# Kernel tuning notes

Measured on AMD Instinct MI355X. Metric: run time of the kernel, lower is better.

## Reference

```python
import jax, jax.numpy as jnp
import numpy as np
from math import sqrt

B, L, D, H, DK, IN = 128, 256, 128, 4, 64, 40
N = B * L
E = 524288
NLAYERS = 4
DISW = 1.5
EPS = 1e-5


def _ln(x, g, b):
    mu = x.mean(-1, keepdims=True)
    v = ((x - mu) ** 2).mean(-1, keepdims=True)
    return (x - mu) / jnp.sqrt(v + EPS) * g + b


def setup_inputs() -> dict:
    key = jax.random.key(0)
    ks = jax.random.split(key, 32)
    x = jax.random.normal(ks[0], (N, IN), jnp.float32)
    # equal-sized graphs: graph g owns nodes [g*L, (g+1)*L)
    e_per = E // B
    off = (jnp.arange(E) // e_per) * L
    src = off + jax.random.randint(ks[1], (E,), 0, L)
    dst = off + jax.random.randint(ks[2], (E,), 0, L)
    edge_index = jnp.stack([src, dst]).astype(jnp.int32)
    edge_attr = jax.random.uniform(ks[3], (E,), jnp.float32)
    # adjacency-type matrix with entries in {0, 1, 1.2} as in the source's adj semantics
    a = jax.random.randint(ks[4], (B, L, L), 0, 3)
    adj = jnp.where(a == 2, 1.2, a.astype(jnp.float32))
    dis = jax.random.randint(ks[5], (B, L, L), 0, 7).astype(jnp.float32)
    mask = jnp.ones((B, L), dtype=bool)  # all graphs have length L -> no padding
    s = 0.05
    p = {}
    p['gnn0_rel_w'] = jax.random.normal(ks[6], (IN, D)) * s
    p['gnn0_rel_b'] = jnp.zeros((D,), jnp.float32)
    p['gnn0_root_w'] = jax.random.normal(ks[7], (IN, D)) * s
    p['gnn_rel_w'] = jax.random.normal(ks[8], (NLAYERS - 1, D, D)) * s
    p['gnn_rel_b'] = jnp.zeros((NLAYERS - 1, D), jnp.float32)
    p['gnn_root_w'] = jax.random.normal(ks[9], (NLAYERS - 1, D, D)) * s
    p['nm_g'] = jnp.ones((NLAYERS, D), jnp.float32)
    p['nm_b'] = jnp.zeros((NLAYERS, D), jnp.float32)
    p['wq'] = jax.random.normal(ks[10], (NLAYERS, D, H * DK)) * s
    p['wk'] = jax.random.normal(ks[11], (NLAYERS, D, H * DK)) * s
    p['wv'] = jax.random.normal(ks[12], (NLAYERS, D, H * DK)) * s
    p['fc'] = jax.random.normal(ks[13], (NLAYERS, H * DK, D)) * s
    p['mha_ln_g'] = jnp.ones((NLAYERS, D), jnp.float32)
    p['mha_ln_b'] = jnp.zeros((NLAYERS, D), jnp.float32)
    p['enc_ln_g'] = jnp.ones((NLAYERS, D), jnp.float32)
    p['enc_ln_b'] = jnp.zeros((NLAYERS, D), jnp.float32)
    p['proj_w'] = jax.random.normal(ks[14], (D, D)) * s
    p['proj_b'] = jnp.zeros((D,), jnp.float32)
    return dict(x=x, edge_index=edge_index, edge_attr=edge_attr, adj=adj, dis=dis, mask=mask, **p)


def _graph_conv(x, src, dst, ew, rel_w, rel_b, root_w):
    # torch_geometric GraphConv: lin_rel(sum_j e_ji * x_j) + lin_root(x_i)
    msg = ew[:, None] * x[src]
    agg = jax.ops.segment_sum(msg, dst, num_segments=N)
    return agg @ rel_w + rel_b + x @ root_w


def _encoder(xb, pad, matrix, wq, wk, wv, fc, mg, mb, eg, eb):
    q = (xb @ wq).reshape(B, L, H, DK).transpose(0, 2, 1, 3)  # [B,H,L,dk]
    k = (xb @ wk).reshape(B, L, H, DK).transpose(0, 2, 1, 3)
    v = (xb @ wv).reshape(B, L, H, DK).transpose(0, 2, 1, 3)
    scores = jnp.einsum('bhqd,bhkd->bhqk', q, k) / sqrt(DK) * matrix[:, None]
    scores = jnp.where(pad[:, None, None, :], -1e9, scores)
    attn = jax.nn.softmax(scores, axis=-1)
    ctx = jnp.einsum('bhqk,bhkd->bhqd', attn, v).transpose(0, 2, 1, 3).reshape(B, L, H * DK)
    out = _ln(ctx @ fc, mg, mb)  # MHA output LayerNorm (dropout is eval -> identity)
    return _ln(out + xb, eg, eb)  # EncoderLayer residual + LayerNorm


def reference(x, edge_index, edge_attr, adj, dis, mask,
              gnn0_rel_w, gnn0_rel_b, gnn0_root_w,
              gnn_rel_w, gnn_rel_b, gnn_root_w,
              nm_g, nm_b, wq, wk, wv, fc,
              mha_ln_g, mha_ln_b, enc_ln_g, enc_ln_b,
              proj_w, proj_b):
    src, dst = edge_index[0], edge_index[1]
    # matrix construction (done once; same matrix_pad reused every layer)
    adj_ = jnp.where(adj == 1.2, 1.1, adj)
    dis_ = jnp.where(dis == 0.0, 0.0, 1.0 / jnp.power(DISW, dis - 1.0))
    matrix = jnp.where(adj == 0.0, dis_, adj_)  # [B,L,L]
    pad = ~mask  # key padding mask (True = masked); all-False here
    h = x
    for i in range(NLAYERS):
        rw = gnn0_rel_w if i == 0 else gnn_rel_w[i - 1]
        rb = gnn0_rel_b if i == 0 else gnn_rel_b[i - 1]
        ow = gnn0_root_w if i == 0 else gnn_root_w[i - 1]
        h = _graph_conv(h, src, dst, edge_attr, rw, rb, ow)
        h = jax.nn.relu(_ln(h, nm_g[i], nm_b[i]))
        xb = h.reshape(B, L, D)  # to_dense_batch with equal lengths
        xb = _encoder(xb, pad, matrix, wq[i], wk[i], wv[i], fc[i],
                      mha_ln_g[i], mha_ln_b[i], enc_ln_g[i], enc_ln_b[i])
        h = xb.reshape(N, D)  # masked_select back to node list
    return h @ proj_w + proj_b
```

## Files before the change

### kernel.cpp

```cpp
#include <hip/hip_runtime.h>
#include <stdint.h>

typedef unsigned short u16;
typedef unsigned int u32;
typedef __attribute__((ext_vector_type(4))) float f32x4;
typedef __attribute__((ext_vector_type(8))) short bf16x8;

#define NB 128
#define LL 256
#define DD 128
#define EDGES 524288
#define EPG 4096
#define NN (NB*LL)

__device__ __forceinline__ float bf2f(u16 u) {
    union { u32 i; float f; } v; v.i = ((u32)u) << 16; return v.f;
}
__device__ __forceinline__ u16 f2bf(float f) {
    union { float f; u32 i; } v; v.f = f;
    u32 i = v.i;
    u32 r = (i + 0x7fffu + ((i >> 16) & 1u)) >> 16;
    return (u16)r;
}
__device__ __forceinline__ float matfn(float a, float dv) {
    if (a != 0.f) return (a == 1.2f) ? 1.1f : a;
    return (dv == 0.f) ? 0.f : exp2f((1.f - dv) * 0.5849625007211562f);
}
__device__ __forceinline__ float red16(float v) {
#pragma unroll
    for (int off = 1; off < 16; off <<= 1) v += __shfl_xor(v, off, 64);
    return v;
}
__device__ __forceinline__ u32 cvtpk(float lo, float hi) {
    u32 r;
    asm("v_cvt_pk_bf16_f32 %0, %1, %2" : "=v"(r) : "v"(lo), "v"(hi));
    return r;
}
__device__ __forceinline__ u32 bperm(int srcLane, u32 v) {
    return (u32)__builtin_amdgcn_ds_bpermute(srcLane << 2, (int)v);
}


__global__ __launch_bounds__(256) void zero_f32(float* __restrict__ p, int n) {
    int i = blockIdx.x * 256 + threadIdx.x;
    if (i < n) p[i] = 0.f;
}

__global__ __launch_bounds__(256) void scatter_w_k(const int* __restrict__ srcI,
                                                   const int* __restrict__ dstI,
                                                   const float* __restrict__ ew,
                                                   float* __restrict__ Wf) {
    int e = blockIdx.x * 256 + threadIdx.x;
    if (e >= EDGES) return;
    int b = e >> 12;
    atomicAdd(&Wf[(size_t)b * 65536 + (size_t)(dstI[e] & 255) * 256 + (srcI[e] & 255)], ew[e]);
}

__global__ __launch_bounds__(256) void cast_w_k(const float* __restrict__ Wf, u16* __restrict__ Wb) {
    int i = blockIdx.x * 256 + threadIdx.x;
    float4 v = ((const float4*)Wf)[i];
    ushort4 o;
    o.x = f2bf(v.x); o.y = f2bf(v.y); o.z = f2bf(v.z); o.w = f2bf(v.w);
    ((ushort4*)Wb)[i] = o;
}

__global__ __launch_bounds__(256) void build_matrix_k(const float* __restrict__ adj,
                                                      const float* __restrict__ dis,
                                                      float* __restrict__ mat) {
    int i = blockIdx.x * 256 + threadIdx.x;
    mat[i] = matfn(adj[i], dis[i]);
}

__global__ __launch_bounds__(256) void prep_weights_k(
        const float* __restrict__ g0_rel_w, const float* __restrict__ g0_root_w,
        const float* __restrict__ g_rel_w,  const float* __restrict__ g_root_w,
        const float* __restrict__ wq, const float* __restrict__ wk,
        const float* __restrict__ wv, const float* __restrict__ fc,
        const float* __restrict__ proj_w,
        u16* __restrict__ wconvT0, u16* __restrict__ wconvT,
        u16* __restrict__ wqkvT, u16* __restrict__ fcT, u16* __restrict__ projT) {
    int i = blockIdx.x * 256 + threadIdx.x;
    if (i < 16384) {
        int m = i >> 7, k = i & 127;
        float v = 0.f;
        if (k < 40) v = g0_rel_w[k * 128 + m];
        else if (k >= 64 && k < 104) v = g0_root_w[(k - 64) * 128 + m];
        wconvT0[i] = f2bf(v);
        return;
    }
    i -= 16384;
    if (i < 98304) {
        int l = i >> 15, jj = i & 32767;
        int m = jj >> 8, k = jj & 255;
        float v = (k < 128) ? g_rel_w[l * 16384 + k * 128 + m]
                            : g_root_w[l * 16384 + (k - 128) * 128 + m];
        wconvT[i] = f2bf(v);
        return;
    }
    i -= 98304;
    if (i < 393216) {
        int l = i / 98304, jj = i % 98304;
        int m = jj >> 7, k = jj & 127;
        const float* s = (m < 256) ? wq : (m < 512) ? wk : wv;
        int mm = m & 255;
        wqkvT[i] = f2bf(s[l * 32768 + k * 256 + mm]);
        return;
    }
    i -= 393216;
    if (i < 131072) {
        int l = i >> 15, jj = i & 32767;
        int m = jj >> 8, k = jj & 255;
        fcT[i] = f2bf(fc[l * 32768 + k * 128 + m]);
        return;
    }
    i -= 131072;
    {
        int m = i >> 7, k = i & 127;
        projT[i] = f2bf(proj_w[k * 128 + m]);
    }
}

template<bool IS0>
__global__ __launch_bounds__(256) void transpose_h_k(const u16* __restrict__ h,
                                                     const float* __restrict__ x,
                                                     u16* __restrict__ hT) {
    int gw = blockIdx.x * 4 + (threadIdx.x >> 6);
    int lane = threadIdx.x & 63;
    int b = gw >> 6, rem = gw & 63, db = rem >> 5, jb = rem & 31;
    int d = (db << 6) + lane;
    u16 vals[8];
#pragma unroll
    for (int jj = 0; jj < 8; ++jj) {
        int node = (b << 8) + (jb << 3) + jj;
        if (IS0) vals[jj] = (d < 40) ? f2bf(x[(size_t)node * 40 + d]) : (u16)0;
        else     vals[jj] = h[(size_t)node * 128 + d];
    }
    *(uint4*)(hT + (size_t)b * 32768 + (size_t)d * 256 + (jb << 3)) = *(uint4*)vals;
}


template<bool IS0>
__global__ __launch_bounds__(256) void gemm_agg(const u16* __restrict__ Wb,
                                                const u16* __restrict__ BT0,
                                                const float* __restrict__ x,
                                                u16* __restrict__ Aagg) {
    __shared__ __align__(16) u16 lds[8192];
    char* ldsc = (char*)lds;
    int t = threadIdx.x, lane = t & 63, wid = t >> 6;
    int b = blockIdx.x >> 1, rt = blockIdx.x & 1;
    int row0 = rt << 7, nbase = b << 8;
    const u16* A = Wb + (size_t)b * 65536 + (size_t)row0 * 256;
    const u16* BT = BT0 + (size_t)b * 32768;

    f32x4 zero = {0.f, 0.f, 0.f, 0.f};
    f32x4 acc[4][4];
#pragma unroll
    for (int mt = 0; mt < 4; ++mt)
#pragma unroll
        for (int nt = 0; nt < 4; ++nt) acc[mt][nt] = zero;

    int wr = wid >> 1, wc = wid & 1;
    int rA = wr * 64 + (lane & 15);
    int rB = wc * 64 + (lane & 15);
    int kch = (lane >> 4) << 4;

    for (int kt = 0; kt < 8; ++kt) {
        int kc = kt << 5;
#pragma unroll
        for (int i = 0; i < 2; ++i) {
            int off = wid * 2048 + i * 1024 + lane * 16;
            int r = off >> 6, cb = off & 63;
            __builtin_amdgcn_global_load_lds((const u32*)((const char*)A + ((size_t)r * 256 + kc) * 2 + cb),
                                             (u32*)(ldsc + wid * 2048 + i * 1024), 16, 0, 0);
            __builtin_amdgcn_global_load_lds((const u32*)((const char*)BT + ((size_t)r * 256 + kc) * 2 + cb),
                                             (u32*)(ldsc + 8192 + wid * 2048 + i * 1024), 16, 0, 0);
        }
        __syncthreads();
        bf16x8 af[4], bfr[4];
#pragma unroll
        for (int mt = 0; mt < 4; ++mt)
            af[mt] = *(const bf16x8*)(ldsc + (rA + mt * 16) * 64 + kch);
#pragma unroll
        for (int nt = 0; nt < 4; ++nt)
            bfr[nt] = *(const bf16x8*)(ldsc + 8192 + (rB + nt * 16) * 64 + kch);
#pragma unroll
        for (int mt = 0; mt < 4; ++mt)
#pragma unroll
            for (int nt = 0; nt < 4; ++nt)
                acc[mt][nt] = __builtin_amdgcn_mfma_f32_16x16x32_bf16(af[mt], bfr[nt], acc[mt][nt], 0, 0, 0);
        __syncthreads();
    }

    int colb = wc * 64 + (lane & 15);
    int rowb = wr * 64 + ((lane >> 4) << 2);
#pragma unroll
    for (int mt = 0; mt < 4; ++mt)
#pragma unroll
        for (int nt = 0; nt < 4; ++nt)
#pragma unroll
            for (int r = 0; r < 4; ++r)
                Aagg[(size_t)(nbase + row0 + rowb + mt * 16 + r) * 128 + colb + nt * 16]
                    = f2bf(acc[mt][nt][r]);
    if (IS0) {
        for (int idx = t; idx < 128 * 40; idx += 256) {
            int i = idx / 40, c = idx - i * 40;
            int node = nbase + row0 + i;
            Aagg[(size_t)node * 128 + 64 + c] = f2bf(x[(size_t)node * 40 + c]);
        }
    }
}


__global__ __launch_bounds__(256) void gemm_qkv(const u16* __restrict__ A,
                                                const u16* __restrict__ BT,
                                                u16* __restrict__ qkv,
                                                u16* __restrict__ vT) {
    __shared__ __align__(16) u16 lds[8192];
    char* ldsc = (char*)lds;
    int t = threadIdx.x, lane = t & 63, wid = t >> 6;
    int row0 = blockIdx.x * 128, col0 = blockIdx.y * 128;

    f32x4 zero = {0.f, 0.f, 0.f, 0.f};
    f32x4 acc[4][4];
#pragma unroll
    for (int mt = 0; mt < 4; ++mt)
#pragma unroll
        for (int nt = 0; nt < 4; ++nt) acc[mt][nt] = zero;

    int wr = wid >> 1, wc = wid & 1;
    int rA = wr * 64 + (lane & 15);
    int rB = wc * 64 + (lane & 15);
    int kch = (lane >> 4) << 4;

    for (int kt = 0; kt < 4; ++kt) {
        int kc = kt << 5;
#pragma unroll
        for (int i = 0; i < 2; ++i) {
            int off = wid * 2048 + i * 1024 + lane * 16;
            int r = off >> 6, cb = off & 63;
            __builtin_amdgcn_global_load_lds((const u32*)((const char*)A + ((size_t)(row0 + r) * 128 + kc) * 2 + cb),
                                             (u32*)(ldsc + wid * 2048 + i * 1024), 16, 0, 0);
            __builtin_amdgcn_global_load_lds((const u32*)((const char*)BT + ((size_t)(col0 + r) * 128 + kc) * 2 + cb),
                                             (u32*)(ldsc + 8192 + wid * 2048 + i * 1024), 16, 0, 0);
        }
        __syncthreads();
        bf16x8 af[4], bfr[4];
#pragma unroll
        for (int mt = 0; mt < 4; ++mt)
            af[mt] = *(const bf16x8*)(ldsc + (rA + mt * 16) * 64 + kch);
#pragma unroll
        for (int nt = 0; nt < 4; ++nt)
            bfr[nt] = *(const bf16x8*)(ldsc + 8192 + (rB + nt * 16) * 64 + kch);
#pragma unroll
        for (int mt = 0; mt < 4; ++mt)
#pragma unroll
            for (int nt = 0; nt < 4; ++nt)
                acc[mt][nt] = __builtin_amdgcn_mfma_f32_16x16x32_bf16(af[mt], bfr[nt], acc[mt][nt], 0, 0, 0);
        __syncthreads();
    }

    int colb = col0 + wc * 64 + (lane & 15);
    int rowb = row0 + wr * 64 + ((lane >> 4) << 2);
    if (col0 < 512) {
#pragma unroll
        for (int mt = 0; mt < 4; ++mt)
#pragma unroll
            for (int nt = 0; nt < 4; ++nt)
#pragma unroll
                for (int r = 0; r < 4; ++r)
                    qkv[(size_t)(rowb + mt * 16 + r) * 768 + colb + nt * 16] = f2bf(acc[mt][nt][r]);
    } else {
        int bb = row0 >> 8;
#pragma unroll
        for (int mt = 0; mt < 4; ++mt) {
            int node0 = (rowb + mt * 16) & 255;
#pragma unroll
            for (int nt = 0; nt < 4; ++nt) {
                int c = colb + nt * 16 - 512;
                int hh = c >> 6, d = c & 63;
                u16 tmp[4];
#pragma unroll
                for (int r = 0; r < 4; ++r) tmp[r] = f2bf(acc[mt][nt][r]);
                *(ushort4*)(vT + (size_t)(bb * 4 + hh) * 16384 + d * 256 + node0) = *(ushort4*)tmp;
            }
        }
    }
}


__global__ __launch_bounds__(256) void gemm_proj(const u16* __restrict__ A,
                                                 const u16* __restrict__ BT,
                                                 float* __restrict__ Out,
                                                 const float* __restrict__ bias) {
    __shared__ __align__(16) u16 lds[8192];
    char* ldsc = (char*)lds;
    int t = threadIdx.x, lane = t & 63, wid = t >> 6;
    int row0 = blockIdx.x * 128;

    f32x4 zero = {0.f, 0.f, 0.f, 0.f};
    f32x4 acc[4][4];
#pragma unroll
    for (int mt = 0; mt < 4; ++mt)
#pragma unroll
        for (int nt = 0; nt < 4; ++nt) acc[mt][nt] = zero;

    int wr = wid >> 1, wc = wid & 1;
    int rA = wr * 64 + (lane & 15);
    int rB = wc * 64 + (lane & 15);
    int kch = (lane >> 4) << 4;

    for (int kt = 0; kt < 4; ++kt) {
        int kc = kt << 5;
#pragma unroll
        for (int i = 0; i < 2; ++i) {
            int off = wid * 2048 + i * 1024 + lane * 16;
            int r = off >> 6, cb = off & 63;
            __builtin_amdgcn_global_load_lds((const u32*)((const char*)A + ((size_t)(row0 + r) * 128 + kc) * 2 + cb),
                                             (u32*)(ldsc + wid * 2048 + i * 1024), 16, 0, 0);
            __builtin_amdgcn_global_load_lds((const u32*)((const char*)BT + ((size_t)r * 128 + kc) * 2 + cb),
                                             (u32*)(ldsc + 8192 + wid * 2048 + i * 1024), 16, 0, 0);
        }
        __syncthreads();
        bf16x8 af[4], bfr[4];
#pragma unroll
        for (int mt = 0; mt < 4; ++mt)
            af[mt] = *(const bf16x8*)(ldsc + (rA + mt * 16) * 64 + kch);
#pragma unroll
        for (int nt = 0; nt < 4; ++nt)
            bfr[nt] = *(const bf16x8*)(ldsc + 8192 + (rB + nt * 16) * 64 + kch);
#pragma unroll
        for (int mt = 0; mt < 4; ++mt)
#pragma unroll
            for (int nt = 0; nt < 4; ++nt)
                acc[mt][nt] = __builtin_amdgcn_mfma_f32_16x16x32_bf16(af[mt], bfr[nt], acc[mt][nt], 0, 0, 0);
        __syncthreads();
    }

    int colb = wc * 64 + (lane & 15);
    int rowb = row0 + wr * 64 + ((lane >> 4) << 2);
#pragma unroll
    for (int mt = 0; mt < 4; ++mt)
#pragma unroll
        for (int nt = 0; nt < 4; ++nt)
#pragma unroll
            for (int r = 0; r < 4; ++r)
                Out[(size_t)(rowb + mt * 16 + r) * 128 + colb + nt * 16] =
                    acc[mt][nt][r] + bias[colb + nt * 16];
}


__global__ __launch_bounds__(256) void gemm_conv_ln0(const u16* __restrict__ A,
                                                     const u16* __restrict__ BT,
                                                     const float* __restrict__ rb,
                                                     const float* __restrict__ g,
                                                     const float* __restrict__ be,
                                                     u16* __restrict__ hout) {
    __shared__ __align__(16) u16 lds[8192];
    char* ldsc = (char*)lds;
    int t = threadIdx.x, lane = t & 63, wid = t >> 6;
    int row0 = blockIdx.x * 128;

    f32x4 zero = {0.f, 0.f, 0.f, 0.f};
    f32x4 acc[4][4];
#pragma unroll
    for (int mt = 0; mt < 4; ++mt)
#pragma unroll
        for (int nt = 0; nt < 4; ++nt) acc[mt][nt] = zero;

    int wr = wid >> 1, wc = wid & 1;
    int rA = wr * 64 + (lane & 15);
    int rB = wc * 64 + (lane & 15);
    int kch = (lane >> 4) << 4;

    for (int kt = 0; kt < 4; ++kt) {
        int kc = kt << 5;
#pragma unroll
        for (int i = 0; i < 2; ++i) {
            int off = wid * 2048 + i * 1024 + lane * 16;
            int r = off >> 6, cb = off & 63;
            __builtin_amdgcn_global_load_lds((const u32*)((const char*)A + ((size_t)(row0 + r) * 128 + kc) * 2 + cb),
                                             (u32*)(ldsc + wid * 2048 + i * 1024), 16, 0, 0);
            __builtin_amdgcn_global_load_lds((const u32*)((const char*)BT + ((size_t)r * 128 + kc) * 2 + cb),
                                             (u32*)(ldsc + 8192 + wid * 2048 + i * 1024), 16, 0, 0);
        }
        __syncthreads();
        bf16x8 af[4], bfr[4];
#pragma unroll
        for (int mt = 0; mt < 4; ++mt)
            af[mt] = *(const bf16x8*)(ldsc + (rA + mt * 16) * 64 + kch);
#pragma unroll
        for (int nt = 0; nt < 4; ++nt)
            bfr[nt] = *(const bf16x8*)(ldsc + 8192 + (rB + nt * 16) * 64 + kch);
#pragma unroll
        for (int mt = 0; mt < 4; ++mt)
#pragma unroll
            for (int nt = 0; nt < 4; ++nt)
                acc[mt][nt] = __builtin_amdgcn_mfma_f32_16x16x32_bf16(af[mt], bfr[nt], acc[mt][nt], 0, 0, 0);
        __syncthreads();
    }

    float* redS = (float*)ldsc;
    float* redQ = (float*)(ldsc + 2048);
    int colbase = wc * 64 + (lane & 15);
    int qrow = (lane >> 4) << 2;
    float rbv[4], gv[4], bev[4];
#pragma unroll
    for (int nt = 0; nt < 4; ++nt) {
        int c = colbase + nt * 16;
        rbv[nt] = rb[c]; gv[nt] = g[c]; bev[nt] = be[c];
    }
#pragma unroll
    for (int mt = 0; mt < 4; ++mt)
#pragma unroll
        for (int r = 0; r < 4; ++r) {
            float s = 0.f, q = 0.f;
#pragma unroll
            for (int nt = 0; nt < 4; ++nt) {
                float v = acc[mt][nt][r] + rbv[nt];
                s += v; q += v * v;
            }
            s = red16(s); q = red16(q);
            if ((lane & 15) == 0) {
                int lr = wr * 64 + qrow + mt * 16 + r;
                redS[lr * 2 + wc] = s; redQ[lr * 2 + wc] = q;
            }
        }
    __syncthreads();
#pragma unroll
    for (int mt = 0; mt < 4; ++mt)
#pragma unroll
        for (int r = 0; r < 4; ++r) {
            int lr = wr * 64 + qrow + mt * 16 + r;
            float mu = (redS[lr * 2] + redS[lr * 2 + 1]) * (1.f / 128.f);
            float var = (redQ[lr * 2] + redQ[lr * 2 + 1]) * (1.f / 128.f) - mu * mu;
            float rs = rsqrtf(var + 1e-5f);
            size_t rbase = (size_t)(row0 + lr) * 128;
#pragma unroll
            for (int nt = 0; nt < 4; ++nt) {
                float v = acc[mt][nt][r] + rbv[nt];
                float o = (v - mu) * rs * gv[nt] + bev[nt];
                o = o < 0.f ? 0.f : o;
                hout[rbase + colbase + nt * 16] = f2bf(o);
            }
        }
}


__global__ __launch_bounds__(256) void gemm_conv_ln_split(const u16* __restrict__ Aagg,
                                                          u16* h,
                                                          const u16* __restrict__ BT,
                                                          const float* __restrict__ rb,
                                                          const float* __restrict__ g,
                                                          const float* __restrict__ be) {
    __shared__ __align__(16) u16 lds[8192];
    char* ldsc = (char*)lds;
    int t = threadIdx.x, lane = t & 63, wid = t >> 6;
    int row0 = blockIdx.x * 128;

    f32x4 zero = {0.f, 0.f, 0.f, 0.f};
    f32x4 acc[4][4];
#pragma unroll
    for (int mt = 0; mt < 4; ++mt)
#pragma unroll
        for (int nt = 0; nt < 4; ++nt) acc[mt][nt] = zero;

    int wr = wid >> 1, wc = wid & 1;
    int rA = wr * 64 + (lane & 15);
    int rB = wc * 64 + (lane & 15);
    int kch = (lane >> 4) << 4;

    for (int kt = 0; kt < 8; ++kt) {
        const u16* Abase = (kt < 4) ? Aagg : (const u16*)h;
        int kcl = (kt & 3) << 5;
        int kc = kt << 5;
#pragma unroll
        for (int i = 0; i < 2; ++i) {
            int off = wid * 2048 + i * 1024 + lane * 16;
            int r = off >> 6, cb = off & 63;
            __builtin_amdgcn_global_load_lds((const u32*)((const char*)Abase + ((size_t)(row0 + r) * 128 + kcl) * 2 + cb),
                                             (u32*)(ldsc + wid * 2048 + i * 1024), 16, 0, 0);
            __builtin_amdgcn_global_load_lds((const u32*)((const char*)BT + ((size_t)r * 256 + kc) * 2 + cb),
                                             (u32*)(ldsc + 8192 + wid * 2048 + i * 1024), 16, 0, 0);
        }
        __syncthreads();
        bf16x8 af[4], bfr[4];
#pragma unroll
        for (int mt = 0; mt < 4; ++mt)
            af[mt] = *(const bf16x8*)(ldsc + (rA + mt * 16) * 64 + kch);
#pragma unroll
        for (int nt = 0; nt < 4; ++nt)
            bfr[nt] = *(const bf16x8*)(ldsc + 8192 + (rB + nt * 16) * 64 + kch);
#pragma unroll
        for (int mt = 0; mt < 4; ++mt)
#pragma unroll
            for (int nt = 0; nt < 4; ++nt)
                acc[mt][nt] = __builtin_amdgcn_mfma_f32_16x16x32_bf16(af[mt], bfr[nt], acc[mt][nt], 0, 0, 0);
        __syncthreads();
    }

    float* redS = (float*)ldsc;
    float* redQ = (float*)(ldsc + 2048);
    int colbase = wc * 64 + (lane & 15);
    int qrow = (lane >> 4) << 2;
    float rbv[4], gv[4], bev[4];
#pragma unroll
    for (int nt = 0; nt < 4; ++nt) {
        int c = colbase + nt * 16;
        rbv[nt] = rb[c]; gv[nt] = g[c]; bev[nt] = be[c];
    }
#pragma unroll
    for (int mt = 0; mt < 4; ++mt)
#pragma unroll
        for (int r = 0; r < 4; ++r) {
            float s = 0.f, q = 0.f;
#pragma unroll
            for (int nt = 0; nt < 4; ++nt) {
                float v = acc[mt][nt][r] + rbv[nt];
                s += v; q += v * v;
            }
            s = red16(s); q = red16(q);
            if ((lane & 15) == 0) {
                int lr = wr * 64 + qrow + mt * 16 + r;
                redS[lr * 2 + wc] = s; redQ[lr * 2 + wc] = q;
            }
        }
    __syncthreads();
#pragma unroll
    for (int mt = 0; mt < 4; ++mt)
#pragma unroll
        for (int r = 0; r < 4; ++r) {
            int lr = wr * 64 + qrow + mt * 16 + r;
            float mu = (redS[lr * 2] + redS[lr * 2 + 1]) * (1.f / 128.f);
            float var = (redQ[lr * 2] + redQ[lr * 2 + 1]) * (1.f / 128.f) - mu * mu;
            float rs = rsqrtf(var + 1e-5f);
            size_t rbase = (size_t)(row0 + lr) * 128;
#pragma unroll
            for (int nt = 0; nt < 4; ++nt) {
                float v = acc[mt][nt][r] + rbv[nt];
                float o = (v - mu) * rs * gv[nt] + bev[nt];
                o = o < 0.f ? 0.f : o;
                h[rbase + colbase + nt * 16] = f2bf(o);
            }
        }
}


__global__ __launch_bounds__(256) void gemm_fc_ln2(const u16* __restrict__ A,
                                                   const u16* __restrict__ BT,
                                                   const float* __restrict__ mg,
                                                   const float* __restrict__ mb,
                                                   const float* __restrict__ eg,
                                                   const float* __restrict__ eb,
                                                   u16* __restrict__ h) {
    __shared__ __align__(16) u16 lds[8192];
    char* ldsc = (char*)lds;
    int t = threadIdx.x, lane = t & 63, wid = t >> 6;
    int row0 = blockIdx.x * 128;

    f32x4 zero = {0.f, 0.f, 0.f, 0.f};
    f32x4 acc[4][4];
#pragma unroll
    for (int mt = 0; mt < 4; ++mt)
#pragma unroll
        for (int nt = 0; nt < 4; ++nt) acc[mt][nt] = zero;

    int wr = wid >> 1, wc = wid & 1;
    int rA = wr * 64 + (lane & 15);
    int rB = wc * 64 + (lane & 15);
    int kch = (lane >> 4) << 4;

    for (int kt = 0; kt < 8; ++kt) {
        int kc = kt << 5;
#pragma unroll
        for (int i = 0; i < 2; ++i) {
            int off = wid * 2048 + i * 1024 + lane * 16;
            int r = off >> 6, cb = off & 63;
            __builtin_amdgcn_global_load_lds((const u32*)((const char*)A + ((size_t)(row0 + r) * 256 + kc) * 2 + cb),
                                             (u32*)(ldsc + wid * 2048 + i * 1024), 16, 0, 0);
            __builtin_amdgcn_global_load_lds((const u32*)((const char*)BT + ((size_t)r * 256 + kc) * 2 + cb),
                                             (u32*)(ldsc + 8192 + wid * 2048 + i * 1024), 16, 0, 0);
        }
        __syncthreads();
        bf16x8 af[4], bfr[4];
#pragma unroll
        for (int mt = 0; mt < 4; ++mt)
            af[mt] = *(const bf16x8*)(ldsc + (rA + mt * 16) * 64 + kch);
#pragma unroll
        for (int nt = 0; nt < 4; ++nt)
            bfr[nt] = *(const bf16x8*)(ldsc + 8192 + (rB + nt * 16) * 64 + kch);
#pragma unroll
        for (int mt = 0; mt < 4; ++mt)
#pragma unroll
            for (int nt = 0; nt < 4; ++nt)
                acc[mt][nt] = __builtin_amdgcn_mfma_f32_16x16x32_bf16(af[mt], bfr[nt], acc[mt][nt], 0, 0, 0);
        __syncthreads();
    }

    float* redS  = (float*)ldsc;
    float* redQ  = (float*)(ldsc + 2048);
    float* redS2 = (float*)(ldsc + 4096);
    float* redQ2 = (float*)(ldsc + 6144);
    int colbase = wc * 64 + (lane & 15);
    int qrow = (lane >> 4) << 2;
    float mgv[4], mbv[4], egv[4], ebv[4];
#pragma unroll
    for (int nt = 0; nt < 4; ++nt) {
        int c = colbase + nt * 16;
        mgv[nt] = mg[c]; mbv[nt] = mb[c]; egv[nt] = eg[c]; ebv[nt] = eb[c];
    }
#pragma unroll
    for (int mt = 0; mt < 4; ++mt)
#pragma unroll
        for (int r = 0; r < 4; ++r) {
            float s = 0.f, q = 0.f;
#pragma unroll
            for (int nt = 0; nt < 4; ++nt) {
                float v = acc[mt][nt][r];
                s += v; q += v * v;
            }
            s = red16(s); q = red16(q);
            if ((lane & 15) == 0) {
                int lr = wr * 64 + qrow + mt * 16 + r;
                redS[lr * 2 + wc] = s; redQ[lr * 2 + wc] = q;
            }
        }
    __syncthreads();
#pragma unroll
    for (int mt = 0; mt < 4; ++mt)
#pragma unroll
        for (int r = 0; r < 4; ++r) {
            int lr = wr * 64 + qrow + mt * 16 + r;
            float mu = (redS[lr * 2] + redS[lr * 2 + 1]) * (1.f / 128.f);
            float var = (redQ[lr * 2] + redQ[lr * 2 + 1]) * (1.f / 128.f) - mu * mu;
            float rs = rsqrtf(var + 1e-5f);
            size_t rbase = (size_t)(row0 + lr) * 128;
            float s2 = 0.f, q2 = 0.f;
#pragma unroll
            for (int nt = 0; nt < 4; ++nt) {
                float o = (acc[mt][nt][r] - mu) * rs * mgv[nt] + mbv[nt];
                float z = o + bf2f(h[rbase + colbase + nt * 16]);
                acc[mt][nt][r] = z;
                s2 += z; q2 += z * z;
            }
            s2 = red16(s2); q2 = red16(q2);
            if ((lane & 15) == 0) {
                redS2[lr * 2 + wc] = s2; redQ2[lr * 2 + wc] = q2;
            }
        }
    __syncthreads();
#pragma unroll
    for (int mt = 0; mt < 4; ++mt)
#pragma unroll
        for (int r = 0; r < 4; ++r) {
            int lr = wr * 64 + qrow + mt * 16 + r;
            float mu = (redS2[lr * 2] + redS2[lr * 2 + 1]) * (1.f / 128.f);
            float var = (redQ2[lr * 2] + redQ2[lr * 2 + 1]) * (1.f / 128.f) - mu * mu;
            float rs = rsqrtf(var + 1e-5f);
            size_t rbase = (size_t)(row0 + lr) * 128;
#pragma unroll
            for (int nt = 0; nt < 4; ++nt) {
                float z = acc[mt][nt][r];
                h[rbase + colbase + nt * 16] = f2bf((z - mu) * rs * egv[nt] + ebv[nt]);
            }
        }
}


__global__ __launch_bounds__(512) void attn_k(const u16* __restrict__ qkv,
                                              const u16* __restrict__ vT,
                                              const float* __restrict__ mat,
                                              u16* __restrict__ ctx) {
    __shared__ __align__(16) u16 Kl[256 * 72];
    __shared__ __align__(16) u16 Vl[64 * 264];
    int t = threadIdx.x, lane = t & 63, w = t >> 6;
    int b = blockIdx.x, hh = blockIdx.y;
    int nbase = b * LL;
    int lg = lane >> 4, q16 = lane & 15;

    if (t < 256) {
        const u16* kb = qkv + (size_t)nbase * 768 + 256 + hh * 64;
#pragma unroll
        for (int i = 0; i < 8; ++i) {
            int idx = i * 256 + t;
            int node = idx >> 3, oct = idx & 7;
            *(uint4*)(Kl + node * 72 + oct * 8) = *(const uint4*)(kb + (size_t)node * 768 + oct * 8);
        }
    } else {
        int tt = t - 256;
        const u16* vsrc = vT + (size_t)(b * 4 + hh) * 16384;
#pragma unroll
        for (int i = 0; i < 8; ++i) {
            int idx = i * 256 + tt;
            int d = idx >> 5, p = idx & 31;
            *(uint4*)(Vl + d * 264 + p * 8) = *(const uint4*)(vsrc + d * 256 + p * 8);
        }
    }
    __syncthreads();

    f32x4 zero = {0.f, 0.f, 0.f, 0.f};
    bool loA = (lg < 2);
    int s01 = q16 + ((lg & 1) << 5);
    int s23 = s01 + 16;

    for (int qi = 0; qi < 2; ++qi) {
        int qrow_l = w * 32 + qi * 16;

        const u16* qsrc = qkv + (size_t)(nbase + qrow_l + q16) * 768 + hh * 64 + (lg << 3);
        bf16x8 aq0 = *(const bf16x8*)(qsrc);
        bf16x8 aq1 = *(const bf16x8*)(qsrc + 32);

        f32x4 sc[16];
#pragma unroll
        for (int nt = 0; nt < 16; ++nt) {
            const u16* ks = Kl + (nt * 16 + q16) * 72 + (lg << 3);
            bf16x8 k0 = *(const bf16x8*)(ks);
            bf16x8 k1 = *(const bf16x8*)(ks + 32);
            f32x4 a = __builtin_amdgcn_mfma_f32_16x16x32_bf16(k0, aq0, zero, 0, 0, 0);
            a = __builtin_amdgcn_mfma_f32_16x16x32_bf16(k1, aq1, a, 0, 0, 0);
            sc[nt] = a;
        }

        const float* mrow = mat + ((size_t)b * LL + qrow_l + q16) * LL + (lg << 2);
#pragma unroll
        for (int nt = 0; nt < 16; ++nt) {
            f32x4 mv = *(const f32x4*)(mrow + nt * 16);
#pragma unroll
            for (int r = 0; r < 4; ++r)
                sc[nt][r] *= 0.125f * mv[r];
        }

        float mx = -1e30f;
#pragma unroll
        for (int nt = 0; nt < 16; ++nt)
#pragma unroll
            for (int r = 0; r < 4; ++r) mx = fmaxf(mx, sc[nt][r]);
        mx = fmaxf(mx, __shfl_xor(mx, 16, 64));
        mx = fmaxf(mx, __shfl_xor(mx, 32, 64));
        float sm = 0.f;
#pragma unroll
        for (int nt = 0; nt < 16; ++nt)
#pragma unroll
            for (int r = 0; r < 4; ++r) {
                float e = __expf(sc[nt][r] - mx);
                sc[nt][r] = e;
                sm += e;
            }
        sm += __shfl_xor(sm, 16, 64);
        sm += __shfl_xor(sm, 32, 64);
        float inv = 1.f / sm;
#pragma unroll
        for (int nt = 0; nt < 16; ++nt)
#pragma unroll
            for (int r = 0; r < 4; ++r) sc[nt][r] *= inv;

        f32x4 oa[4];
#pragma unroll
        for (int dt = 0; dt < 4; ++dt) oa[dt] = zero;
#pragma unroll
        for (int kt = 0; kt < 8; ++kt) {
            u32 A0 = cvtpk(sc[2 * kt][0], sc[2 * kt][1]);
            u32 A1 = cvtpk(sc[2 * kt][2], sc[2 * kt][3]);
            u32 B0 = cvtpk(sc[2 * kt + 1][0], sc[2 * kt + 1][1]);
            u32 B1 = cvtpk(sc[2 * kt + 1][2], sc[2 * kt + 1][3]);
            u32 a0s = bperm(s01, A0), b0s = bperm(s01, B0);
            u32 a1s = bperm(s01, A1), b1s = bperm(s01, B1);
            u32 a0t = bperm(s23, A0), b0t = bperm(s23, B0);
            u32 a1t = bperm(s23, A1), b1t = bperm(s23, B1);
            union { u32 u[4]; bf16x8 v; } pa;
            pa.u[0] = loA ? a0s : b0s;
            pa.u[1] = loA ? a1s : b1s;
            pa.u[2] = loA ? a0t : b0t;
            pa.u[3] = loA ? a1t : b1t;
#pragma unroll
            for (int dt = 0; dt < 4; ++dt) {
                bf16x8 bv = *(const bf16x8*)(Vl + (dt * 16 + q16) * 264 + kt * 32 + (lg << 3));
                oa[dt] = __builtin_amdgcn_mfma_f32_16x16x32_bf16(pa.v, bv, oa[dt], 0, 0, 0);
            }
        }
#pragma unroll
        for (int dt = 0; dt < 4; ++dt)
#pragma unroll
            for (int r = 0; r < 4; ++r)
                ctx[(size_t)(nbase + qrow_l + (lg << 2) + r) * 256 + hh * 64 + dt * 16 + q16] = f2bf(oa[dt][r]);
    }
}


extern "C" void kernel_launch(void* const* d_in, const int* in_sizes, int n_in,
                              void* d_out, int out_size, void* d_ws, size_t ws_size,
                              hipStream_t stream) {
    (void)out_size; (void)ws_size; (void)n_in;
    const float* x        = (const float*)d_in[0];
    const int*   ei       = (const int*)d_in[1];
    const float* ea       = (const float*)d_in[2];
    const float* adj      = (const float*)d_in[3];
    const float* dis      = (const float*)d_in[4];
    int pb = (in_sizes[5] == 5120) ? 5 : 6;
    const float* g0_rel_w = (const float*)d_in[pb + 0];
    const float* g0_rel_b = (const float*)d_in[pb + 1];
    const float* g0_root_w= (const float*)d_in[pb + 2];
    const float* g_rel_w  = (const float*)d_in[pb + 3];
    const float* g_rel_b  = (const float*)d_in[pb + 4];
    const float* g_root_w = (const float*)d_in[pb + 5];
    const float* nm_g     = (const float*)d_in[pb + 6];
    const float* nm_b     = (const float*)d_in[pb + 7];
    const float* wq       = (const float*)d_in[pb + 8];
    const float* wk       = (const float*)d_in[pb + 9];
    const float* wv       = (const float*)d_in[pb + 10];
    const float* fc       = (const float*)d_in[pb + 11];
    const float* mha_g    = (const float*)d_in[pb + 12];
    const float* mha_b    = (const float*)d_in[pb + 13];
    const float* enc_g    = (const float*)d_in[pb + 14];
    const float* enc_b    = (const float*)d_in[pb + 15];
    const float* proj_w   = (const float*)d_in[pb + 16];
    const float* proj_b   = (const float*)d_in[pb + 17];
    const int* srcI = ei;
    const int* dstI = ei + EDGES;

    char* w = (char*)d_ws;
    float* Wf     = (float*)w; w += (size_t)33554432;
    u16*   Acat   = (u16*)w;   w += (size_t)16777216;
    u16*   h      = (u16*)w;   w += (size_t)8388608;
    u16*   qkv    = (u16*)w;   w += (size_t)50331648;
    u16*   Wb     = (u16*)w;   w += (size_t)16777216;
    u16*   bigT   = (u16*)w;   w += (size_t)16777216;
    u16* wconvT0  = (u16*)w;   w += (size_t)32768;
    u16* wconvT   = (u16*)w;   w += (size_t)196608;
    u16* wqkvT    = (u16*)w;   w += (size_t)786432;
    u16* fcT      = (u16*)w;   w += (size_t)262144;
    u16* projT    = (u16*)w;   w += (size_t)32768;
    float* mat = Wf;
    u16*   ctx = Acat;
    u16*   hT  = bigT;
    u16*   vT  = bigT;

    zero_f32<<<32768, 256, 0, stream>>>(Wf, 8388608);
    scatter_w_k<<<2048, 256, 0, stream>>>(srcI, dstI, ea, Wf);
    cast_w_k<<<8192, 256, 0, stream>>>(Wf, Wb);
    build_matrix_k<<<32768, 256, 0, stream>>>(adj, dis, mat);
    prep_weights_k<<<2560, 256, 0, stream>>>(g0_rel_w, g0_root_w, g_rel_w, g_root_w,
                                             wq, wk, wv, fc, proj_w,
                                             wconvT0, wconvT, wqkvT, fcT, projT);

    for (int L = 0; L < 4; ++L) {
        if (L == 0) {
            transpose_h_k<true><<<2048, 256, 0, stream>>>(h, x, hT);
            gemm_agg<true><<<256, 256, 0, stream>>>(Wb, hT, x, Acat);
            gemm_conv_ln0<<<256, 256, 0, stream>>>(Acat, wconvT0, g0_rel_b, nm_g, nm_b, h);
        } else {
            transpose_h_k<false><<<2048, 256, 0, stream>>>(h, x, hT);
            gemm_agg<false><<<256, 256, 0, stream>>>(Wb, hT, x, Acat);
            gemm_conv_ln_split<<<256, 256, 0, stream>>>(Acat, h, wconvT + (L - 1) * 32768,
                                                        g_rel_b + (L - 1) * 128,
                                                        nm_g + L * 128, nm_b + L * 128);
        }
        gemm_qkv<<<dim3(256, 6), 256, 0, stream>>>(h, wqkvT + L * 98304, qkv, vT);
        attn_k<<<dim3(NB, 4), 512, 0, stream>>>(qkv, vT, mat, ctx);
        gemm_fc_ln2<<<256, 256, 0, stream>>>(ctx, fcT + L * 32768,
                                             mha_g + L * 128, mha_b + L * 128,
                                             enc_g + L * 128, enc_b + L * 128, h);
    }
    gemm_proj<<<256, 256, 0, stream>>>(h, projT, (float*)d_out, proj_b);
}
```

Measured before the change: 548.5 us.

## Fuse h transpose into fc-LN epilogue and store Q/K head-major

The per-layer transpose kernels for h are removed: the fc+LayerNorm epilogue now also writes the transposed bf16 activations that the next layer's aggregation GEMM consumes. Only the layer-0 transpose of x remains, run once before the loop. The QKV GEMM writes Q and K into per-(graph, head) contiguous buffers, so the attention kernel loads K tiles and Q rows with simpler, denser addressing. The 1/sqrt(dk) scale is folded into the precomputed attention matrix, and the zeroing kernel becomes a hipMemsetAsync. The cost is scattered 16-bit stores in the QKV epilogue and extra transposed stores in the fc epilogue.

```diff
diff --git a/kernel.cpp b/kernel.cpp
--- a/kernel.cpp
+++ b/kernel.cpp
@@ -40,11 +40,6 @@
     return (u32)__builtin_amdgcn_ds_bpermute(srcLane << 2, (int)v);
 }
 
-
-__global__ __launch_bounds__(256) void zero_f32(float* __restrict__ p, int n) {
-    int i = blockIdx.x * 256 + threadIdx.x;
-    if (i < n) p[i] = 0.f;
-}
 
 __global__ __launch_bounds__(256) void scatter_w_k(const int* __restrict__ srcI,
                                                    const int* __restrict__ dstI,
@@ -68,7 +63,7 @@
                                                       const float* __restrict__ dis,
                                                       float* __restrict__ mat) {
     int i = blockIdx.x * 256 + threadIdx.x;
-    mat[i] = matfn(adj[i], dis[i]);
+    mat[i] = 0.125f * matfn(adj[i], dis[i]);
 }
 
 __global__ __launch_bounds__(256) void prep_weights_k(
@@ -120,9 +115,7 @@
     }
 }
 
-template<bool IS0>
-__global__ __launch_bounds__(256) void transpose_h_k(const u16* __restrict__ h,
-                                                     const float* __restrict__ x,
+__global__ __launch_bounds__(256) void transpose_x_k(const float* __restrict__ x,
                                                      u16* __restrict__ hT) {
     int gw = blockIdx.x * 4 + (threadIdx.x >> 6);
     int lane = threadIdx.x & 63;
@@ -132,8 +125,7 @@
 #pragma unroll
     for (int jj = 0; jj < 8; ++jj) {
         int node = (b << 8) + (jb << 3) + jj;
-        if (IS0) vals[jj] = (d < 40) ? f2bf(x[(size_t)node * 40 + d]) : (u16)0;
-        else     vals[jj] = h[(size_t)node * 128 + d];
+        vals[jj] = (d < 40) ? f2bf(x[(size_t)node * 40 + d]) : (u16)0;
     }
     *(uint4*)(hT + (size_t)b * 32768 + (size_t)d * 256 + (jb << 3)) = *(uint4*)vals;
 }
@@ -213,7 +205,8 @@
 
 __global__ __launch_bounds__(256) void gemm_qkv(const u16* __restrict__ A,
                                                 const u16* __restrict__ BT,
-                                                u16* __restrict__ qkv,
+                                                u16* __restrict__ qP,
+                                                u16* __restrict__ kP,
                                                 u16* __restrict__ vT) {
     __shared__ __align__(16) u16 lds[8192];
     char* ldsc = (char*)lds;
@@ -261,16 +254,23 @@
 
     int colb = col0 + wc * 64 + (lane & 15);
     int rowb = row0 + wr * 64 + ((lane >> 4) << 2);
+    int bb = row0 >> 8;
     if (col0 < 512) {
-#pragma unroll
-        for (int mt = 0; mt < 4; ++mt)
-#pragma unroll
-            for (int nt = 0; nt < 4; ++nt)
-#pragma unroll
-                for (int r = 0; r < 4; ++r)
-                    qkv[(size_t)(rowb + mt * 16 + r) * 768 + colb + nt * 16] = f2bf(acc[mt][nt][r]);
+        u16* dst = (col0 < 256) ? qP : kP;
+#pragma unroll
+        for (int mt = 0; mt < 4; ++mt) {
+#pragma unroll
+            for (int nt = 0; nt < 4; ++nt) {
+                int c = (colb + nt * 16) & 255;
+                int hh = c >> 6, d = c & 63;
+#pragma unroll
+                for (int r = 0; r < 4; ++r) {
+                    int node = (rowb + mt * 16 + r) & 255;
+                    dst[(size_t)(bb * 4 + hh) * 16384 + node * 64 + d] = f2bf(acc[mt][nt][r]);
+                }
+            }
+        }
     } else {
-        int bb = row0 >> 8;
 #pragma unroll
         for (int mt = 0; mt < 4; ++mt) {
             int node0 = (rowb + mt * 16) & 255;
@@ -551,7 +551,8 @@
                                                    const float* __restrict__ mb,
                                                    const float* __restrict__ eg,
                                                    const float* __restrict__ eb,
-                                                   u16* __restrict__ h) {
+                                                   u16* __restrict__ h,
+                                                   u16* __restrict__ hT) {
     __shared__ __align__(16) u16 lds[8192];
     char* ldsc = (char*)lds;
     int t = threadIdx.x, lane = t & 63, wid = t >> 6;
@@ -648,8 +649,10 @@
             }
         }
     __syncthreads();
-#pragma unroll
-    for (int mt = 0; mt < 4; ++mt)
+    int bb = row0 >> 8;
+#pragma unroll
+    for (int mt = 0; mt < 4; ++mt) {
+        u16 tvals[4][4];
 #pragma unroll
         for (int r = 0; r < 4; ++r) {
             int lr = wr * 64 + qrow + mt * 16 + r;
@@ -660,13 +663,23 @@
 #pragma unroll
             for (int nt = 0; nt < 4; ++nt) {
                 float z = acc[mt][nt][r];
-                h[rbase + colbase + nt * 16] = f2bf((z - mu) * rs * egv[nt] + ebv[nt]);
-            }
-        }
-}
-
-
-__global__ __launch_bounds__(512) void attn_k(const u16* __restrict__ qkv,
+                u16 o = f2bf((z - mu) * rs * egv[nt] + ebv[nt]);
+                h[rbase + colbase + nt * 16] = o;
+                tvals[nt][r] = o;
+            }
+        }
+        int node0 = ((row0 & 255) + wr * 64 + qrow + mt * 16);
+#pragma unroll
+        for (int nt = 0; nt < 4; ++nt) {
+            int d = colbase + nt * 16;
+            *(ushort4*)(hT + (size_t)bb * 32768 + (size_t)d * 256 + node0) = *(ushort4*)tvals[nt];
+        }
+    }
+}
+
+
+__global__ __launch_bounds__(512) void attn_k(const u16* __restrict__ qP,
+                                              const u16* __restrict__ kP,
                                               const u16* __restrict__ vT,
                                               const float* __restrict__ mat,
                                               u16* __restrict__ ctx) {
@@ -674,25 +687,23 @@
     __shared__ __align__(16) u16 Vl[64 * 264];
     int t = threadIdx.x, lane = t & 63, w = t >> 6;
     int b = blockIdx.x, hh = blockIdx.y;
-    int nbase = b * LL;
+    int bh = b * 4 + hh;
     int lg = lane >> 4, q16 = lane & 15;
 
-    if (t < 256) {
-        const u16* kb = qkv + (size_t)nbase * 768 + 256 + hh * 64;
-#pragma unroll
-        for (int i = 0; i < 8; ++i) {
-            int idx = i * 256 + t;
+    {
+        const u16* kb = kP + (size_t)bh * 16384;
+#pragma unroll
+        for (int i = 0; i < 4; ++i) {
+            int idx = i * 512 + t;
             int node = idx >> 3, oct = idx & 7;
-            *(uint4*)(Kl + node * 72 + oct * 8) = *(const uint4*)(kb + (size_t)node * 768 + oct * 8);
-        }
-    } else {
-        int tt = t - 256;
-        const u16* vsrc = vT + (size_t)(b * 4 + hh) * 16384;
-#pragma unroll
-        for (int i = 0; i < 8; ++i) {
-            int idx = i * 256 + tt;
+            *(uint4*)(Kl + node * 72 + oct * 8) = *(const uint4*)(kb + node * 64 + oct * 8);
+        }
+        const u16* vb = vT + (size_t)bh * 16384;
+#pragma unroll
+        for (int i = 0; i < 4; ++i) {
+            int idx = i * 512 + t;
             int d = idx >> 5, p = idx & 31;
-            *(uint4*)(Vl + d * 264 + p * 8) = *(const uint4*)(vsrc + d * 256 + p * 8);
+            *(uint4*)(Vl + d * 264 + p * 8) = *(const uint4*)(vb + d * 256 + p * 8);
         }
     }
     __syncthreads();
@@ -705,7 +716,7 @@
     for (int qi = 0; qi < 2; ++qi) {
         int qrow_l = w * 32 + qi * 16;
 
-        const u16* qsrc = qkv + (size_t)(nbase + qrow_l + q16) * 768 + hh * 64 + (lg << 3);
+        const u16* qsrc = qP + (size_t)bh * 16384 + (qrow_l + q16) * 64 + (lg << 3);
         bf16x8 aq0 = *(const bf16x8*)(qsrc);
         bf16x8 aq1 = *(const bf16x8*)(qsrc + 32);
 
@@ -726,7 +737,7 @@
             f32x4 mv = *(const f32x4*)(mrow + nt * 16);
 #pragma unroll
             for (int r = 0; r < 4; ++r)
-                sc[nt][r] *= 0.125f * mv[r];
+                sc[nt][r] *= mv[r];
         }
 
         float mx = -1e30f;
@@ -781,7 +792,7 @@
         for (int dt = 0; dt < 4; ++dt)
 #pragma unroll
             for (int r = 0; r < 4; ++r)
-                ctx[(size_t)(nbase + qrow_l + (lg << 2) + r) * 256 + hh * 64 + dt * 16 + q16] = f2bf(oa[dt][r]);
+                ctx[(size_t)(b * LL + qrow_l + (lg << 2) + r) * 256 + hh * 64 + dt * 16 + q16] = f2bf(oa[dt][r]);
     }
 }
 
@@ -821,7 +832,8 @@
     float* Wf     = (float*)w; w += (size_t)33554432;
     u16*   Acat   = (u16*)w;   w += (size_t)16777216;
     u16*   h      = (u16*)w;   w += (size_t)8388608;
-    u16*   qkv    = (u16*)w;   w += (size_t)50331648;
+    u16*   qP     = (u16*)w;   w += (size_t)16777216;
+    u16*   kP     = (u16*)w;   w += (size_t)16777216;
     u16*   Wb     = (u16*)w;   w += (size_t)16777216;
     u16*   bigT   = (u16*)w;   w += (size_t)16777216;
     u16* wconvT0  = (u16*)w;   w += (size_t)32768;
@@ -834,31 +846,30 @@
     u16*   hT  = bigT;
     u16*   vT  = bigT;
 
-    zero_f32<<<32768, 256, 0, stream>>>(Wf, 8388608);
+    hipMemsetAsync(Wf, 0, 33554432, stream);
     scatter_w_k<<<2048, 256, 0, stream>>>(srcI, dstI, ea, Wf);
     cast_w_k<<<8192, 256, 0, stream>>>(Wf, Wb);
     build_matrix_k<<<32768, 256, 0, stream>>>(adj, dis, mat);
     prep_weights_k<<<2560, 256, 0, stream>>>(g0_rel_w, g0_root_w, g_rel_w, g_root_w,
                                              wq, wk, wv, fc, proj_w,
                                              wconvT0, wconvT, wqkvT, fcT, projT);
+    transpose_x_k<<<2048, 256, 0, stream>>>(x, hT);
 
     for (int L = 0; L < 4; ++L) {
         if (L == 0) {
-            transpose_h_k<true><<<2048, 256, 0, stream>>>(h, x, hT);
             gemm_agg<true><<<256, 256, 0, stream>>>(Wb, hT, x, Acat);
             gemm_conv_ln0<<<256, 256, 0, stream>>>(Acat, wconvT0, g0_rel_b, nm_g, nm_b, h);
         } else {
-            transpose_h_k<false><<<2048, 256, 0, stream>>>(h, x, hT);
             gemm_agg<false><<<256, 256, 0, stream>>>(Wb, hT, x, Acat);
             gemm_conv_ln_split<<<256, 256, 0, stream>>>(Acat, h, wconvT + (L - 1) * 32768,
                                                         g_rel_b + (L - 1) * 128,
                                                         nm_g + L * 128, nm_b + L * 128);
         }
-        gemm_qkv<<<dim3(256, 6), 256, 0, stream>>>(h, wqkvT + L * 98304, qkv, vT);
-        attn_k<<<dim3(NB, 4), 512, 0, stream>>>(qkv, vT, mat, ctx);
+        gemm_qkv<<<dim3(256, 6), 256, 0, stream>>>(h, wqkvT + L * 98304, qP, kP, vT);
+        attn_k<<<dim3(NB, 4), 512, 0, stream>>>(qP, kP, vT, mat, ctx);
         gemm_fc_ln2<<<256, 256, 0, stream>>>(ctx, fcT + L * 32768,
                                              mha_g + L * 128, mha_b + L * 128,
-                                             enc_g + L * 128, enc_b + L * 128, h);
+                                             enc_g + L * 128, enc_b + L * 128, h, hT);
     }
     gemm_proj<<<256, 256, 0, stream>>>(h, projT, (float*)d_out, proj_b);
 }
```

After: 521.6 us. -4.9%, faster.
